# Optimization experiments

Hardware: AMD Instinct MI355X
Metric: run time of the kernel (lower is better)

Reference implementation:

```python
import jax, jax.numpy as jnp
import numpy as np

B, C, H, W = 8, 16, 256, 256
D = C - 4  # hidden channels
N = H * W


def _grid_edges(h, w):
    idx = np.arange(h * w).reshape(h, w)
    right = np.stack([idx[:, :-1].ravel(), idx[:, 1:].ravel()])
    down = np.stack([idx[:-1, :].ravel(), idx[1:, :].ravel()])
    e = np.concatenate([right, down], axis=1)
    # both directions (undirected 4-neighborhood)
    return np.concatenate([e, e[::-1]], axis=1).astype(np.int64)


def setup_inputs() -> dict:
    key = jax.random.key(0)
    ks = jax.random.split(key, 12)
    s = lambda *sh: 1.0 / np.sqrt(np.prod(sh[1:]))
    inp = {
        "x": jax.random.normal(ks[0], (B, C, H, W), jnp.float32),
        "edge_index": jnp.asarray(_grid_edges(H, W)),
        "steps": 8,
        # hidden_update: Conv2d(D, D, 3, padding=1)
        "Wh": jax.random.normal(ks[1], (D, D, 3, 3), jnp.float32) * s(D, D * 9),
        "bh": jnp.zeros((D,), jnp.float32),
        # graph message passing linear (D -> D)
        "Wmp": jax.random.normal(ks[2], (D, D), jnp.float32) * s(D, D),
        "bmp": jnp.zeros((D,), jnp.float32),
        # alive_update: Conv2d(D, 1, 1)
        "Wa": jax.random.normal(ks[3], (1, D), jnp.float32) * s(1, D),
        "ba": jnp.zeros((1,), jnp.float32),
        # rgb_decode: Conv2d(D+1, D, 1) -> ReLU -> Conv2d(D, 3, 1)
        "Wr1": jax.random.normal(ks[4], (D, D + 1), jnp.float32) * s(D, D + 1),
        "br1": jnp.zeros((D,), jnp.float32),
        "Wr2": jax.random.normal(ks[5], (3, D), jnp.float32) * s(3, D),
        "br2": jnp.zeros((3,), jnp.float32),
    }
    return inp


def _conv1x1(x, w, b):
    # x: [B,Ci,H,W], w: [Co,Ci]
    return jnp.einsum("bchw,oc->bohw", x, w) + b[None, :, None, None]


def _graph_mp(hidden, edge_index, Wmp, bmp, deg_inv):
    # hidden: [B,D,H,W] -> nodes [B,N,D]
    b, d, h, w = hidden.shape
    nodes = hidden.reshape(b, d, h * w).transpose(0, 2, 1)
    src, dst = edge_index[0], edge_index[1]
    msg = nodes[:, src] @ Wmp.T + bmp  # [B,E,D]
    agg = jnp.zeros_like(nodes).at[:, dst].add(msg)  # scatter-add
    agg = agg * deg_inv[None, :, None]  # mean aggregation
    return agg.transpose(0, 2, 1).reshape(b, d, h, w)


def reference(x, edge_index, steps, Wh, bh, Wmp, bmp, Wa, ba, Wr1, br1, Wr2, br2):
    n = x.shape[2] * x.shape[3]
    deg = jnp.zeros((n,), x.dtype).at[edge_index[1]].add(1.0)
    deg_inv = 1.0 / jnp.maximum(deg, 1.0)
    for _ in range(steps):
        hidden = x[:, 4:]
        h_local = jax.lax.conv_general_dilated(
            hidden, Wh, (1, 1), ((1, 1), (1, 1)),
            dimension_numbers=("NCHW", "OIHW", "NCHW"),
        ) + bh[None, :, None, None]
        h_graph = _graph_mp(hidden, edge_index, Wmp, bmp, deg_inv)
        hidden_new = jax.nn.elu(hidden + h_local + h_graph)
        alive_new = jax.nn.sigmoid(_conv1x1(hidden_new, Wa, ba))
        cat = jnp.concatenate([hidden_new, alive_new], axis=1)
        rgb_new = jax.nn.sigmoid(_conv1x1(jax.nn.relu(_conv1x1(cat, Wr1, br1)), Wr2, br2))
        rgb_new = rgb_new * alive_new
        x = jnp.concatenate([alive_new, rgb_new, hidden_new], axis=1)
    return x
```

## Files before the change

### kernel.cpp

```cpp
#include <hip/hip_runtime.h>
#include <math.h>

#define Wd 256
#define Hd 256
#define Nd (Wd*Hd)
#define Bd 8

__device__ __forceinline__ int imax(int a, int b) { return a > b ? a : b; }
__device__ __forceinline__ int imin(int a, int b) { return a < b ? a : b; }

__global__ __launch_bounds__(256) void nca_prep(
    const float* __restrict__ Wh, const float* __restrict__ bh,
    const float* __restrict__ Wmp, const float* __restrict__ bmp,
    float* __restrict__ wtab)
{
    int idx = blockIdx.x * 256 + threadIdx.x;
    if (idx < 1728) {
        int i = idx / 144, rem = idx % 144, o = rem / 12, k = rem % 12;
        float v = 0.0f;
        if (k < 9) {
            v = Wh[(o * 12 + i) * 9 + k];
            if (k == 4 && o == i) v += 1.0f;
        } else if (k == 9) {
            v = Wmp[o * 12 + i];
        }
        wtab[idx] = v;
    } else if (idx < 1740) {
        int o = idx - 1728;
        wtab[idx] = bh[o] + bmp[o];
    }
}

__global__ __launch_bounds__(256, 2) void nca_step(
    const float* __restrict__ src, int sbs, int soff, int maxidx,
    float* __restrict__ dst, const float* __restrict__ wtab)
{
    const int tid = threadIdx.x;
    const int bx = blockIdx.x, by = blockIdx.y, b = blockIdx.z;
    const int tx = tid & 7, ty = tid >> 3;
    const int gx0 = bx * 32 + tx * 4;
    const int gy  = by * 32 + ty;

    const bool vT = gy > 0, vB = gy < Hd - 1;
    const bool vL = gx0 > 0, vR = gx0 < Wd - 4;

    const int yT = vT ? gy - 1 : 0;
    const int yB = vB ? gy + 1 : Hd - 1;

    float dinv[4];
    #pragma unroll
    for (int p = 0; p < 4; ++p) {
        int gx = gx0 + p;
        int deg = (gx > 0) + (gx < Wd - 1) + vT + vB;
        dinv[p] = 1.0f / (float)deg;
    }

    const int base = b * sbs + soff + gx0;
    const int oT = base + yT * Wd;
    const int oM = base + gy * Wd;
    const int oB = base + yB * Wd;

    const float* bias = wtab + 1728;
    float acc[4][12];
    #pragma unroll
    for (int o = 0; o < 12; ++o) {
        float bv = bias[o];
        #pragma unroll
        for (int p = 0; p < 4; ++p) acc[p][o] = bv;
    }

    #pragma unroll 2
    for (int i = 0; i < 12; ++i) {
        const int iT = oT + i * Nd, iM = oM + i * Nd, iB = oB + i * Nd;
        float2 LT = *(const float2*)(src + imax(iT - 2, 0));
        float4 CT = *(const float4*)(src + iT);
        float2 RT = *(const float2*)(src + imin(iT + 4, maxidx - 2));
        float2 LM = *(const float2*)(src + imax(iM - 2, 0));
        float4 CM = *(const float4*)(src + iM);
        float2 RM = *(const float2*)(src + imin(iM + 4, maxidx - 2));
        float2 LB = *(const float2*)(src + imax(iB - 2, 0));
        float4 CB = *(const float4*)(src + iB);
        float2 RB = *(const float2*)(src + imin(iB + 4, maxidx - 2));

        float eT[6], eM[6], eB[6];
        eT[0] = (vT && vL) ? LT.y : 0.0f;
        eT[1] = vT ? CT.x : 0.0f; eT[2] = vT ? CT.y : 0.0f;
        eT[3] = vT ? CT.z : 0.0f; eT[4] = vT ? CT.w : 0.0f;
        eT[5] = (vT && vR) ? RT.x : 0.0f;
        eM[0] = vL ? LM.y : 0.0f;
        eM[1] = CM.x; eM[2] = CM.y; eM[3] = CM.z; eM[4] = CM.w;
        eM[5] = vR ? RM.x : 0.0f;
        eB[0] = (vB && vL) ? LB.y : 0.0f;
        eB[1] = vB ? CB.x : 0.0f; eB[2] = vB ? CB.y : 0.0f;
        eB[3] = vB ? CB.z : 0.0f; eB[4] = vB ? CB.w : 0.0f;
        eB[5] = (vB && vR) ? RB.x : 0.0f;

        float ns[4];
        #pragma unroll
        for (int p = 0; p < 4; ++p)
            ns[p] = (eT[p + 1] + eB[p + 1] + eM[p] + eM[p + 2]) * dinv[p];

        const float4* w4 = (const float4*)(wtab + i * 144);
        #pragma unroll
        for (int o = 0; o < 12; ++o) {
            float4 wa = w4[o * 3 + 0];
            float4 wb = w4[o * 3 + 1];
            float4 wc = w4[o * 3 + 2];
            #pragma unroll
            for (int p = 0; p < 4; ++p) {
                float a = acc[p][o];
                a = fmaf(wa.x, eT[p],     a);
                a = fmaf(wa.y, eT[p + 1], a);
                a = fmaf(wa.z, eT[p + 2], a);
                a = fmaf(wa.w, eM[p],     a);
                a = fmaf(wb.x, eM[p + 1], a);
                a = fmaf(wb.y, eM[p + 2], a);
                a = fmaf(wb.z, eB[p],     a);
                a = fmaf(wb.w, eB[p + 1], a);
                a = fmaf(wc.x, eB[p + 2], a);
                a = fmaf(wc.y, ns[p],     a);
                acc[p][o] = a;
            }
        }
    }

    float* dp = dst + (long)b * (12L * Nd) + (long)gy * Wd + gx0;
    #pragma unroll
    for (int o = 0; o < 12; ++o) {
        float e[4];
        #pragma unroll
        for (int p = 0; p < 4; ++p) {
            float a = acc[p][o];
            e[p] = a > 0.0f ? a : (__expf(a) - 1.0f);
        }
        *(float4*)&dp[(long)o * Nd] = make_float4(e[0], e[1], e[2], e[3]);
    }
}

__global__ __launch_bounds__(256) void nca_final(
    const float* __restrict__ hsrc, float* __restrict__ out,
    const float* __restrict__ Wa, const float* __restrict__ ba,
    const float* __restrict__ Wr1, const float* __restrict__ br1,
    const float* __restrict__ Wr2, const float* __restrict__ br2)
{
    int p = blockIdx.x * 256 + threadIdx.x;
    int b = blockIdx.y;
    const float* hp = hsrc + (long)b * 12 * Nd + p;
    float h[12];
    #pragma unroll
    for (int c = 0; c < 12; ++c) h[c] = hp[(long)c * Nd];

    float za = ba[0];
    #pragma unroll
    for (int c = 0; c < 12; ++c) za = fmaf(Wa[c], h[c], za);
    float alive = 1.0f / (1.0f + __expf(-za));

    float r1[12];
    #pragma unroll
    for (int o = 0; o < 12; ++o) {
        float z = br1[o];
        #pragma unroll
        for (int c = 0; c < 12; ++c) z = fmaf(Wr1[o * 13 + c], h[c], z);
        z = fmaf(Wr1[o * 13 + 12], alive, z);
        r1[o] = fmaxf(z, 0.0f);
    }

    float* op = out + (long)b * 16 * Nd + p;
    op[0] = alive;
    #pragma unroll
    for (int j = 0; j < 3; ++j) {
        float z = br2[j];
        #pragma unroll
        for (int o = 0; o < 12; ++o) z = fmaf(Wr2[j * 12 + o], r1[o], z);
        op[(long)(1 + j) * Nd] = (1.0f / (1.0f + __expf(-z))) * alive;
    }
    #pragma unroll
    for (int c = 0; c < 12; ++c) op[(long)(4 + c) * Nd] = h[c];
}

extern "C" void kernel_launch(void* const* d_in, const int* in_sizes, int n_in,
                              void* d_out, int out_size, void* d_ws, size_t ws_size,
                              hipStream_t stream) {
    const float* x   = (const float*)d_in[0];
    const float* Wh  = (const float*)d_in[3];
    const float* bh  = (const float*)d_in[4];
    const float* Wmp = (const float*)d_in[5];
    const float* bmp = (const float*)d_in[6];
    const float* Wa  = (const float*)d_in[7];
    const float* ba  = (const float*)d_in[8];
    const float* Wr1 = (const float*)d_in[9];
    const float* br1 = (const float*)d_in[10];
    const float* Wr2 = (const float*)d_in[11];
    const float* br2 = (const float*)d_in[12];

    float* bufA = (float*)d_out;
    float* bufB = (float*)d_ws;
    float* wtab = (float*)d_out + 12L * Nd * Bd;

    nca_prep<<<dim3(7), dim3(256), 0, stream>>>(Wh, bh, Wmp, bmp, wtab);

    dim3 grid(8, 8, 8), block(256);
    const int sb16 = 16 * Nd, sb12 = 12 * Nd;
    const int mx1 = 16 * Nd * Bd, mx = 12 * Nd * Bd;
    nca_step<<<grid, block, 0, stream>>>(x,    sb16, 4 * Nd, mx1, bufA, wtab);
    nca_step<<<grid, block, 0, stream>>>(bufA, sb12, 0,      mx,  bufB, wtab);
    nca_step<<<grid, block, 0, stream>>>(bufB, sb12, 0,      mx,  bufA, wtab);
    nca_step<<<grid, block, 0, stream>>>(bufA, sb12, 0,      mx,  bufB, wtab);
    nca_step<<<grid, block, 0, stream>>>(bufB, sb12, 0,      mx,  bufA, wtab);
    nca_step<<<grid, block, 0, stream>>>(bufA, sb12, 0,      mx,  bufB, wtab);
    nca_step<<<grid, block, 0, stream>>>(bufB, sb12, 0,      mx,  bufA, wtab);
    nca_step<<<grid, block, 0, stream>>>(bufA, sb12, 0,      mx,  bufB, wtab);
    nca_final<<<dim3(Nd / 256, Bd), dim3(256), 0, stream>>>(bufB, (float*)d_out,
                                                            Wa, ba, Wr1, br1, Wr2, br2);
}
```

Baseline: 346.5 us.

## Stage halo input tile and weights in shared memory for stencil step

Each block now cooperatively loads a zero-padded 34x34 halo tile for all 12 hidden channels into LDS, plus the combined weight table, then computes the 3x3 conv plus neighbor-mean from LDS. This removes redundant overlapping global loads and boundary clamping per thread. It adds a serialized scalar tile fill, a block barrier and large LDS use, and moves uniform weight reads from the scalar path to LDS.

Result: slower. 450.1 us (+29.9%).

```diff
diff --git a/kernel.cpp b/kernel.cpp
--- a/kernel.cpp
+++ b/kernel.cpp
@@ -5,9 +5,6 @@
 #define Hd 256
 #define Nd (Wd*Hd)
 #define Bd 8
-
-__device__ __forceinline__ int imax(int a, int b) { return a > b ? a : b; }
-__device__ __forceinline__ int imin(int a, int b) { return a < b ? a : b; }
 
 __global__ __launch_bounds__(256) void nca_prep(
     const float* __restrict__ Wh, const float* __restrict__ bh,
@@ -32,93 +29,100 @@
 }
 
 __global__ __launch_bounds__(256, 2) void nca_step(
-    const float* __restrict__ src, int sbs, int soff, int maxidx,
+    const float* __restrict__ src, int sbs, int soff,
     float* __restrict__ dst, const float* __restrict__ wtab)
 {
+    __shared__ float tile[12 * 34 * 36];
+    __shared__ float wlds[1740];
+
     const int tid = threadIdx.x;
     const int bx = blockIdx.x, by = blockIdx.y, b = blockIdx.z;
+    const int x0 = bx * 32, y0 = by * 32;
+    const float* sp = src + b * sbs + soff;
+
+    for (int idx = tid; idx < 1740; idx += 256) wlds[idx] = wtab[idx];
+
+    int jr[5], jc[5]; bool jv[5];
+    #pragma unroll
+    for (int k = 0; k < 5; ++k) {
+        int j = tid + k * 256;
+        jv[k] = j < 1156;
+        jr[k] = j / 34; jc[k] = j % 34;
+    }
+    #pragma unroll 1
+    for (int c = 0; c < 12; ++c) {
+        const float* cp = sp + c * Nd;
+        #pragma unroll
+        for (int k = 0; k < 5; ++k) {
+            if (jv[k]) {
+                int gy = y0 + jr[k] - 1, gx = x0 + jc[k] - 1;
+                float v = 0.0f;
+                if ((unsigned)gy < 256u && (unsigned)gx < 256u) v = cp[gy * Wd + gx];
+                tile[c * 1224 + jr[k] * 36 + jc[k]] = v;
+            }
+        }
+    }
+    __syncthreads();
+
     const int tx = tid & 7, ty = tid >> 3;
-    const int gx0 = bx * 32 + tx * 4;
-    const int gy  = by * 32 + ty;
-
-    const bool vT = gy > 0, vB = gy < Hd - 1;
-    const bool vL = gx0 > 0, vR = gx0 < Wd - 4;
-
-    const int yT = vT ? gy - 1 : 0;
-    const int yB = vB ? gy + 1 : Hd - 1;
+    const int px0 = tx * 4;
+    const int gx0 = x0 + px0, gy = y0 + ty;
 
     float dinv[4];
     #pragma unroll
     for (int p = 0; p < 4; ++p) {
         int gx = gx0 + p;
-        int deg = (gx > 0) + (gx < Wd - 1) + vT + vB;
+        int deg = (gx > 0) + (gx < Wd - 1) + (gy > 0) + (gy < Hd - 1);
         dinv[p] = 1.0f / (float)deg;
     }
 
-    const int base = b * sbs + soff + gx0;
-    const int oT = base + yT * Wd;
-    const int oM = base + gy * Wd;
-    const int oB = base + yB * Wd;
-
-    const float* bias = wtab + 1728;
     float acc[4][12];
     #pragma unroll
     for (int o = 0; o < 12; ++o) {
-        float bv = bias[o];
+        float bv = wlds[1728 + o];
         #pragma unroll
         for (int p = 0; p < 4; ++p) acc[p][o] = bv;
     }
 
-    #pragma unroll 2
+    #pragma unroll 1
     for (int i = 0; i < 12; ++i) {
-        const int iT = oT + i * Nd, iM = oM + i * Nd, iB = oB + i * Nd;
-        float2 LT = *(const float2*)(src + imax(iT - 2, 0));
-        float4 CT = *(const float4*)(src + iT);
-        float2 RT = *(const float2*)(src + imin(iT + 4, maxidx - 2));
-        float2 LM = *(const float2*)(src + imax(iM - 2, 0));
-        float4 CM = *(const float4*)(src + iM);
-        float2 RM = *(const float2*)(src + imin(iM + 4, maxidx - 2));
-        float2 LB = *(const float2*)(src + imax(iB - 2, 0));
-        float4 CB = *(const float4*)(src + iB);
-        float2 RB = *(const float2*)(src + imin(iB + 4, maxidx - 2));
-
-        float eT[6], eM[6], eB[6];
-        eT[0] = (vT && vL) ? LT.y : 0.0f;
-        eT[1] = vT ? CT.x : 0.0f; eT[2] = vT ? CT.y : 0.0f;
-        eT[3] = vT ? CT.z : 0.0f; eT[4] = vT ? CT.w : 0.0f;
-        eT[5] = (vT && vR) ? RT.x : 0.0f;
-        eM[0] = vL ? LM.y : 0.0f;
-        eM[1] = CM.x; eM[2] = CM.y; eM[3] = CM.z; eM[4] = CM.w;
-        eM[5] = vR ? RM.x : 0.0f;
-        eB[0] = (vB && vL) ? LB.y : 0.0f;
-        eB[1] = vB ? CB.x : 0.0f; eB[2] = vB ? CB.y : 0.0f;
-        eB[3] = vB ? CB.z : 0.0f; eB[4] = vB ? CB.w : 0.0f;
-        eB[5] = (vB && vR) ? RB.x : 0.0f;
-
+        const int base = i * 1224 + ty * 36 + px0;
+        float e0[6], e1[6], e2[6];
+        {
+            float4 A0 = *(const float4*)&tile[base];
+            float2 B0 = *(const float2*)&tile[base + 4];
+            float4 A1 = *(const float4*)&tile[base + 36];
+            float2 B1 = *(const float2*)&tile[base + 40];
+            float4 A2 = *(const float4*)&tile[base + 72];
+            float2 B2 = *(const float2*)&tile[base + 76];
+            e0[0]=A0.x; e0[1]=A0.y; e0[2]=A0.z; e0[3]=A0.w; e0[4]=B0.x; e0[5]=B0.y;
+            e1[0]=A1.x; e1[1]=A1.y; e1[2]=A1.z; e1[3]=A1.w; e1[4]=B1.x; e1[5]=B1.y;
+            e2[0]=A2.x; e2[1]=A2.y; e2[2]=A2.z; e2[3]=A2.w; e2[4]=B2.x; e2[5]=B2.y;
+        }
         float ns[4];
         #pragma unroll
         for (int p = 0; p < 4; ++p)
-            ns[p] = (eT[p + 1] + eB[p + 1] + eM[p] + eM[p + 2]) * dinv[p];
-
-        const float4* w4 = (const float4*)(wtab + i * 144);
+            ns[p] = (e0[p + 1] + e2[p + 1] + e1[p] + e1[p + 2]) * dinv[p];
+
+        const int wb = i * 144;
         #pragma unroll
         for (int o = 0; o < 12; ++o) {
-            float4 wa = w4[o * 3 + 0];
-            float4 wb = w4[o * 3 + 1];
-            float4 wc = w4[o * 3 + 2];
+            float4 wa = *(const float4*)&wlds[wb + o * 12];
+            float4 wbv = *(const float4*)&wlds[wb + o * 12 + 4];
+            float4 wc = *(const float4*)&wlds[wb + o * 12 + 8];
             #pragma unroll
             for (int p = 0; p < 4; ++p) {
                 float a = acc[p][o];
-                a = fmaf(wa.x, eT[p],     a);
-                a = fmaf(wa.y, eT[p + 1], a);
-                a = fmaf(wa.z, eT[p + 2], a);
-                a = fmaf(wa.w, eM[p],     a);
-                a = fmaf(wb.x, eM[p + 1], a);
-                a = fmaf(wb.y, eM[p + 2], a);
-                a = fmaf(wb.z, eB[p],     a);
-                a = fmaf(wb.w, eB[p + 1], a);
-                a = fmaf(wc.x, eB[p + 2], a);
-                a = fmaf(wc.y, ns[p],     a);
+                a = fmaf(wa.x, e0[p],     a);
+                a = fmaf(wa.y, e0[p + 1], a);
+                a = fmaf(wa.z, e0[p + 2], a);
+                a = fmaf(wa.w, e1[p],     a);
+                a = fmaf(wbv.x, e1[p + 1], a);
+                a = fmaf(wbv.y, e1[p + 2], a);
+                a = fmaf(wbv.z, e2[p],     a);
+                a = fmaf(wbv.w, e2[p + 1], a);
+                a = fmaf(wc.x,  e2[p + 2], a);
+                a = fmaf(wc.y,  ns[p],     a);
                 acc[p][o] = a;
             }
         }
@@ -201,15 +205,14 @@
 
     dim3 grid(8, 8, 8), block(256);
     const int sb16 = 16 * Nd, sb12 = 12 * Nd;
-    const int mx1 = 16 * Nd * Bd, mx = 12 * Nd * Bd;
-    nca_step<<<grid, block, 0, stream>>>(x,    sb16, 4 * Nd, mx1, bufA, wtab);
-    nca_step<<<grid, block, 0, stream>>>(bufA, sb12, 0,      mx,  bufB, wtab);
-    nca_step<<<grid, block, 0, stream>>>(bufB, sb12, 0,      mx,  bufA, wtab);
-    nca_step<<<grid, block, 0, stream>>>(bufA, sb12, 0,      mx,  bufB, wtab);
-    nca_step<<<grid, block, 0, stream>>>(bufB, sb12, 0,      mx,  bufA, wtab);
-    nca_step<<<grid, block, 0, stream>>>(bufA, sb12, 0,      mx,  bufB, wtab);
-    nca_step<<<grid, block, 0, stream>>>(bufB, sb12, 0,      mx,  bufA, wtab);
-    nca_step<<<grid, block, 0, stream>>>(bufA, sb12, 0,      mx,  bufB, wtab);
+    nca_step<<<grid, block, 0, stream>>>(x,    sb16, 4 * Nd, bufA, wtab);
+    nca_step<<<grid, block, 0, stream>>>(bufA, sb12, 0,      bufB, wtab);
+    nca_step<<<grid, block, 0, stream>>>(bufB, sb12, 0,      bufA, wtab);
+    nca_step<<<grid, block, 0, stream>>>(bufA, sb12, 0,      bufB, wtab);
+    nca_step<<<grid, block, 0, stream>>>(bufB, sb12, 0,      bufA, wtab);
+    nca_step<<<grid, block, 0, stream>>>(bufA, sb12, 0,      bufB, wtab);
+    nca_step<<<grid, block, 0, stream>>>(bufB, sb12, 0,      bufA, wtab);
+    nca_step<<<grid, block, 0, stream>>>(bufA, sb12, 0,      bufB, wtab);
     nca_final<<<dim3(Nd / 256, Bd), dim3(256), 0, stream>>>(bufB, (float*)d_out,
                                                             Wa, ba, Wr1, br1, Wr2, br2);
 }
```
